# Performance work log

Measured on AMD Instinct MI355X. Metric: run time of the kernel, lower is better.

Reference implementation:

```python
import jax, jax.numpy as jnp
import numpy as np

B, T, D = 8, 2048, 512


def setup_inputs() -> dict:
    key = jax.random.key(0)
    ks = jax.random.split(key, 12)
    s = 1.0 / np.sqrt(D)
    return {
        "x": jax.random.normal(ks[0], (B, T, D), dtype=jnp.float32),
        "Wq": jax.random.normal(ks[1], (D, D), dtype=jnp.float32) * s,
        "bq": jax.random.normal(ks[2], (D,), dtype=jnp.float32) * 0.01,
        "Wk": jax.random.normal(ks[3], (D, D), dtype=jnp.float32) * s,
        "bk": jax.random.normal(ks[4], (D,), dtype=jnp.float32) * 0.01,
        "Wv": jax.random.normal(ks[5], (D, D), dtype=jnp.float32) * s,
        "bv": jax.random.normal(ks[6], (D,), dtype=jnp.float32) * 0.01,
        "Wbeta": jax.random.normal(ks[7], (1, D), dtype=jnp.float32) * s,
        "bbeta": jax.random.normal(ks[8], (1,), dtype=jnp.float32) * 0.01,
        "Wo": jax.random.normal(ks[9], (D, D), dtype=jnp.float32) * s,
        "bo": jax.random.normal(ks[10], (D,), dtype=jnp.float32) * 0.01,
    }


def _l2_normalize(v, eps=1e-12):
    # torch F.normalize(p=2, dim=-1): v / max(||v||, eps)
    n = jnp.sqrt(jnp.sum(v * v, axis=-1, keepdims=True))
    return v / jnp.maximum(n, eps)


def _deltanet(x, Wq, bq, Wk, bk, Wv, bv, Wbeta, bbeta, Wo, bo):
    Q = x @ Wq.T + bq                      # [B,T,D]
    K = _l2_normalize(x @ Wk.T + bk)       # [B,T,D], unit-norm keys
    V = x @ Wv.T + bv                      # [B,T,D]
    Beta = jax.nn.sigmoid(K @ Wbeta.T + bbeta)  # [B,T,1]

    # time-major for scan: [T,B,D] / [T,B,1]
    Qt = jnp.swapaxes(Q, 0, 1)
    Kt = jnp.swapaxes(K, 0, 1)
    Vt = jnp.swapaxes(V, 0, 1)
    Bt = jnp.swapaxes(Beta, 0, 1)

    S0 = jnp.zeros((x.shape[0], x.shape[-1], x.shape[-1]), dtype=x.dtype)

    def step(S, inp):
        q, k, v, beta = inp                 # [B,D],[B,D],[B,D],[B,1]
        Sk = jnp.einsum("bij,bj->bi", S, k)           # S k_t
        b = beta[:, :, None]                            # [B,1,1]
        # S_t = S - beta (S k) k^T + beta v k^T
        S = S - b * (Sk[:, :, None] * k[:, None, :]) + b * (v[:, :, None] * k[:, None, :])
        o = jnp.einsum("bij,bj->bi", S, q)              # o_t = S_t q_t
        return S, o

    _, Ot = jax.lax.scan(step, S0, (Qt, Kt, Vt, Bt))    # [T,B,D]
    O = jnp.swapaxes(Ot, 0, 1)                          # [B,T,D]
    return O @ Wo.T + bo


def reference(x, Wq, bq, Wk, bk, Wv, bv, Wbeta, bbeta, Wo, bo):
    return _deltanet(x, Wq, bq, Wk, bk, Wv, bv, Wbeta, bbeta, Wo, bo)
```

## Files before the change

### kernel.cpp

```cpp
#include <hip/hip_runtime.h>

#define D 512
#define T 2048
#define BATCH 8
#define M_ROWS (BATCH*T)
#define CHK 64
#define NCHB 32
#define NCHUNK 256

typedef __attribute__((ext_vector_type(8))) short short8;
typedef __attribute__((ext_vector_type(4))) float floatx4;

__device__ __forceinline__ unsigned short f2bf(float f) {
  unsigned int u = __float_as_uint(f);
  u += 0x7FFFu + ((u >> 16) & 1u);
  return (unsigned short)(u >> 16);
}
__device__ __forceinline__ float bf2f(unsigned int h) {
  return __uint_as_float(h << 16);
}
__device__ __forceinline__ float wave_allreduce(float v) {
  #pragma unroll
  for (int m = 32; m; m >>= 1) v += __shfl_xor(v, m, 64);
  return v;
}
__device__ __forceinline__ void unpack8(uint4 r, float f[8]) {
  f[0] = bf2f(r.x & 0xffffu); f[1] = bf2f(r.x >> 16);
  f[2] = bf2f(r.y & 0xffffu); f[3] = bf2f(r.y >> 16);
  f[4] = bf2f(r.z & 0xffffu); f[5] = bf2f(r.z >> 16);
  f[6] = bf2f(r.w & 0xffffu); f[7] = bf2f(r.w >> 16);
}

typedef const __attribute__((address_space(1))) void* gas_ptr;
typedef __attribute__((address_space(3))) void* lds_ptr;
__device__ __forceinline__ void gld16(const void* g, void* l) {
  __builtin_amdgcn_global_load_lds((gas_ptr)g, (lds_ptr)l, 16, 0, 0);
}

__global__ __launch_bounds__(256) void cast_all(
    const float* __restrict__ x,
    const float* __restrict__ Wq, const float* __restrict__ Wk,
    const float* __restrict__ Wv, const float* __restrict__ Wo,
    unsigned short* __restrict__ Xb, unsigned short* __restrict__ Wqb) {
  int blk = blockIdx.x;
  const float* src;
  unsigned short* dst;
  int idx;
  if (blk < 4096) {
    src = x; dst = Xb; idx = blk * 2048 + threadIdx.x * 8;
  } else {
    int b2 = blk - 4096;
    int sel = b2 >> 7;
    src = (sel == 0) ? Wq : (sel == 1) ? Wk : (sel == 2) ? Wv : Wo;
    dst = Wqb + (size_t)sel * (D * D);
    idx = (b2 & 127) * 2048 + threadIdx.x * 8;
  }
  const float4* sp = (const float4*)(src + idx);
  float4 a = sp[0], b = sp[1];
  uint4 o;
  o.x = f2bf(a.x) | ((unsigned)f2bf(a.y) << 16);
  o.y = f2bf(a.z) | ((unsigned)f2bf(a.w) << 16);
  o.z = f2bf(b.x) | ((unsigned)f2bf(b.y) << 16);
  o.w = f2bf(b.z) | ((unsigned)f2bf(b.w) << 16);
  *(uint4*)(dst + idx) = o;
}

#define BM 128
#define BN 128
#define BK 32

template<bool OUT_BF16>
__global__ __launch_bounds__(256) void gemm_nt(
    const unsigned short* __restrict__ A, const unsigned short* __restrict__ Bw,
    const float* __restrict__ bias, void* __restrict__ Cout, int M, int N, int K)
{
  __shared__ __align__(16) unsigned short As[BM * BK];
  __shared__ __align__(16) unsigned short Bs[BN * BK];
  int tid  = threadIdx.x;
  int lane = tid & 63;
  int wave = tid >> 6;
  int waveM = (wave >> 1) * 64;
  int waveN = (wave & 1) * 64;
  int lrow = lane & 15;
  int quad = lane >> 4;

  floatx4 acc[4][4];
  #pragma unroll
  for (int a_ = 0; a_ < 4; ++a_)
    #pragma unroll
    for (int b_ = 0; b_ < 4; ++b_) acc[a_][b_] = (floatx4){0.f, 0.f, 0.f, 0.f};

  const unsigned short* Ap = A  + (size_t)(blockIdx.y * BM) * K;
  const unsigned short* Bp = Bw + (size_t)(blockIdx.x * BN) * K;
  int r0 = tid >> 2;
  int c0 = (tid & 3) * 8;

  unsigned short* AsW = As + (wave << 9);
  unsigned short* BsW = Bs + (wave << 9);
  const unsigned short* ApL = Ap + (size_t)r0 * K + c0;
  const unsigned short* ApH = Ap + (size_t)(r0 + 64) * K + c0;
  const unsigned short* BpL = Bp + (size_t)r0 * K + c0;
  const unsigned short* BpH = Bp + (size_t)(r0 + 64) * K + c0;

  for (int k0 = 0; k0 < K; k0 += BK) {
    __syncthreads();
    gld16(ApL + k0, AsW);
    gld16(ApH + k0, AsW + 2048);
    gld16(BpL + k0, BsW);
    gld16(BpH + k0, BsW + 2048);
    __syncthreads();
    short8 af[4], bf[4];
    #pragma unroll
    for (int mt = 0; mt < 4; ++mt)
      af[mt] = *(const short8*)&As[(waveM + mt * 16 + lrow) * BK + quad * 8];
    #pragma unroll
    for (int nt = 0; nt < 4; ++nt)
      bf[nt] = *(const short8*)&Bs[(waveN + nt * 16 + lrow) * BK + quad * 8];
    #pragma unroll
    for (int mt = 0; mt < 4; ++mt)
      #pragma unroll
      for (int nt = 0; nt < 4; ++nt)
        acc[mt][nt] = __builtin_amdgcn_mfma_f32_16x16x32_bf16(af[mt], bf[nt], acc[mt][nt], 0, 0, 0);
  }

  int cm = blockIdx.y * BM + waveM;
  int cn = blockIdx.x * BN + waveN;
  #pragma unroll
  for (int nt = 0; nt < 4; ++nt) {
    int col = cn + nt * 16 + lrow;
    float bv = bias[col];
    #pragma unroll
    for (int mt = 0; mt < 4; ++mt) {
      #pragma unroll
      for (int r = 0; r < 4; ++r) {
        int row = cm + mt * 16 + quad * 4 + r;
        float v = acc[mt][nt][r] + bv;
        if (OUT_BF16) ((unsigned short*)Cout)[(size_t)row * N + col] = f2bf(v);
        else          ((float*)Cout)[(size_t)row * N + col] = v;
      }
    }
  }
}

__global__ __launch_bounds__(256) void gemm_qkv(
    const unsigned short* __restrict__ A, const unsigned short* __restrict__ Bw,
    const float* __restrict__ bq, const float* __restrict__ bk,
    const float* __restrict__ bv, unsigned short* __restrict__ Cout)
{
  __shared__ __align__(16) unsigned short As[BM * BK];
  __shared__ __align__(16) unsigned short Bs[BN * BK];
  const int K = D;
  int tid  = threadIdx.x;
  int lane = tid & 63;
  int wave = tid >> 6;
  int waveM = (wave >> 1) * 64;
  int waveN = (wave & 1) * 64;
  int lrow = lane & 15;
  int quad = lane >> 4;

  int mat = blockIdx.x >> 2;
  const float* bias = (mat == 0) ? bq : (mat == 1 ? bk : bv);

  floatx4 acc[4][4];
  #pragma unroll
  for (int a_ = 0; a_ < 4; ++a_)
    #pragma unroll
    for (int b_ = 0; b_ < 4; ++b_) acc[a_][b_] = (floatx4){0.f, 0.f, 0.f, 0.f};

  const unsigned short* Ap = A  + (size_t)(blockIdx.y * BM) * K;
  const unsigned short* Bp = Bw + (size_t)(blockIdx.x * BN) * K;
  int r0 = tid >> 2;
  int c0 = (tid & 3) * 8;

  unsigned short* AsW = As + (wave << 9);
  unsigned short* BsW = Bs + (wave << 9);
  const unsigned short* ApL = Ap + (size_t)r0 * K + c0;
  const unsigned short* ApH = Ap + (size_t)(r0 + 64) * K + c0;
  const unsigned short* BpL = Bp + (size_t)r0 * K + c0;
  const unsigned short* BpH = Bp + (size_t)(r0 + 64) * K + c0;

  for (int k0 = 0; k0 < K; k0 += BK) {
    __syncthreads();
    gld16(ApL + k0, AsW);
    gld16(ApH + k0, AsW + 2048);
    gld16(BpL + k0, BsW);
    gld16(BpH + k0, BsW + 2048);
    __syncthreads();
    short8 af[4], bf[4];
    #pragma unroll
    for (int mt = 0; mt < 4; ++mt)
      af[mt] = *(const short8*)&As[(waveM + mt * 16 + lrow) * BK + quad * 8];
    #pragma unroll
    for (int nt = 0; nt < 4; ++nt)
      bf[nt] = *(const short8*)&Bs[(waveN + nt * 16 + lrow) * BK + quad * 8];
    #pragma unroll
    for (int mt = 0; mt < 4; ++mt)
      #pragma unroll
      for (int nt = 0; nt < 4; ++nt)
        acc[mt][nt] = __builtin_amdgcn_mfma_f32_16x16x32_bf16(af[mt], bf[nt], acc[mt][nt], 0, 0, 0);
  }

  unsigned short* outb = Cout + (size_t)mat * ((size_t)M_ROWS * D);
  int cm = blockIdx.y * BM + waveM;
  int cnl = (blockIdx.x & 3) * BN + waveN;
  #pragma unroll
  for (int nt = 0; nt < 4; ++nt) {
    int col = cnl + nt * 16 + lrow;
    float bvv = bias[col];
    #pragma unroll
    for (int mt = 0; mt < 4; ++mt) {
      #pragma unroll
      for (int r = 0; r < 4; ++r) {
        int row = cm + mt * 16 + quad * 4 + r;
        outb[(size_t)row * D + col] = f2bf(acc[mt][nt][r] + bvv);
      }
    }
  }
}

__global__ __launch_bounds__(256) void norm_beta_kernel(
    unsigned short* __restrict__ Kb, const float* __restrict__ Wbeta,
    const float* __restrict__ bbeta, float* __restrict__ Beta)
{
  int w = blockIdx.x * 4 + (threadIdx.x >> 6);
  int lane = threadIdx.x & 63;
  unsigned short* kp = Kb + (size_t)w * D + lane * 8;
  uint4 raw = *(uint4*)kp;
  float kv[8]; unpack8(raw, kv);
  float ss = 0.f;
  #pragma unroll
  for (int m = 0; m < 8; ++m) ss += kv[m] * kv[m];
  ss = wave_allreduce(ss);
  float inv = 1.0f / fmaxf(sqrtf(ss), 1e-12f);
  const float* wb = Wbeta + lane * 8;
  float dotp = 0.f;
  #pragma unroll
  for (int m = 0; m < 8; ++m) { kv[m] *= inv; dotp += kv[m] * wb[m]; }
  uint4 o;
  o.x = f2bf(kv[0]) | ((unsigned)f2bf(kv[1]) << 16);
  o.y = f2bf(kv[2]) | ((unsigned)f2bf(kv[3]) << 16);
  o.z = f2bf(kv[4]) | ((unsigned)f2bf(kv[5]) << 16);
  o.w = f2bf(kv[6]) | ((unsigned)f2bf(kv[7]) << 16);
  *(uint4*)kp = o;
  dotp = wave_allreduce(dotp);
  if (lane == 0) Beta[w] = 1.0f / (1.0f + expf(-(dotp + bbeta[0])));
}

__global__ __launch_bounds__(256) void transpose_kv(
    const unsigned short* __restrict__ Kb, const unsigned short* __restrict__ Vb,
    unsigned short* __restrict__ KT, unsigned short* __restrict__ VT)
{
  __shared__ __align__(16) unsigned short Kc[64 * 520];
  int cb = blockIdx.x & 255, tid = threadIdx.x;
  const unsigned short* src = (blockIdx.x < 256 ? Kb : Vb) + (size_t)cb * 64 * 512;
  unsigned short* dst = (blockIdx.x < 256 ? KT : VT) + (size_t)cb * 32768;
  #pragma unroll
  for (int it = 0; it < 16; ++it) {
    int e = it * 2048 + tid * 8;
    int row = e >> 9, col = e & 511;
    *(uint4*)&Kc[row * 520 + col] = *(const uint4*)&src[row * 512 + col];
  }
  __syncthreads();
  #pragma unroll
  for (int it = 0; it < 16; ++it) {
    int e = it * 2048 + tid * 8;
    int dk = e >> 6, t0 = e & 63;
    uint4 o;
    unsigned short tv[8];
    #pragma unroll
    for (int u = 0; u < 8; ++u) tv[u] = Kc[(t0 + u) * 520 + dk];
    o.x = tv[0] | ((unsigned)tv[1] << 16);
    o.y = tv[2] | ((unsigned)tv[3] << 16);
    o.z = tv[4] | ((unsigned)tv[5] << 16);
    o.w = tv[6] | ((unsigned)tv[7] << 16);
    *(uint4*)&dst[e] = o;
  }
}

__global__ __launch_bounds__(256) void gram_kernel(
    const unsigned short* __restrict__ Qb, const unsigned short* __restrict__ Kb,
    const float* __restrict__ Beta, float* __restrict__ Abuf,
    unsigned short* __restrict__ Msb)
{
  int cb = blockIdx.x, tid = threadIdx.x, lane = tid & 63, w = tid >> 6;
  int lr = lane & 15, quad = lane >> 4;
  const unsigned short* kc = Kb + (size_t)cb * 64 * 512;
  const unsigned short* qc = Qb + (size_t)cb * 64 * 512;
  floatx4 accK[4], accQ[4];
  #pragma unroll
  for (int nt = 0; nt < 4; ++nt) { accK[nt] = (floatx4){0,0,0,0}; accQ[nt] = (floatx4){0,0,0,0}; }
  #pragma unroll
  for (int ks = 0; ks < 16; ++ks) {
    short8 ak = *(const short8*)&kc[(w * 16 + lr) * 512 + ks * 32 + quad * 8];
    short8 aq = *(const short8*)&qc[(w * 16 + lr) * 512 + ks * 32 + quad * 8];
    short8 bk[4];
    #pragma unroll
    for (int nt = 0; nt < 4; ++nt)
      bk[nt] = *(const short8*)&kc[(nt * 16 + lr) * 512 + ks * 32 + quad * 8];
    #pragma unroll
    for (int nt = 0; nt < 4; ++nt) {
      accK[nt] = __builtin_amdgcn_mfma_f32_16x16x32_bf16(ak, bk[nt], accK[nt], 0, 0, 0);
      accQ[nt] = __builtin_amdgcn_mfma_f32_16x16x32_bf16(aq, bk[nt], accQ[nt], 0, 0, 0);
    }
  }
  #pragma unroll
  for (int nt = 0; nt < 4; ++nt)
    #pragma unroll
    for (int r = 0; r < 4; ++r) {
      int t = w * 16 + quad * 4 + r;
      int j = nt * 16 + lr;
      float bt = Beta[cb * 64 + t];
      Abuf[(size_t)cb * 4096 + t * 64 + j] = (j < t) ? bt * accK[nt][r] : 0.f;
      Msb[(size_t)cb * 4096 + t * 64 + j]  = f2bf((j <= t) ? accQ[nt][r] : 0.f);
    }
}

__global__ __launch_bounds__(64) void tinv_kernel(
    const float* __restrict__ Abuf, const float* __restrict__ Beta,
    unsigned short* __restrict__ Tib)
{
  __shared__ float AB[64 * 64];
  __shared__ float XT[64 * 68];
  int lane = threadIdx.x;
  int cb = blockIdx.x;
  float bl = Beta[cb * 64 + lane];
  const float* Ab = Abuf + (size_t)cb * 4096;
  unsigned short* To = Tib + (size_t)cb * 4096;
  #pragma unroll
  for (int it = 0; it < 16; ++it) {
    int idx = it * 256 + lane * 4;
    *(float4*)&AB[idx] = *(const float4*)&Ab[idx];
  }
  float* Xr = XT + lane * 68;
  #pragma unroll
  for (int j = 0; j < 68; j += 4) *(float4*)&Xr[j] = (float4){0.f,0.f,0.f,0.f};
  for (int t = 0; t < 64; ++t) {
    const float* Ar = AB + t * 64;
    float p0 = 0.f, p1 = 0.f, p2 = 0.f, p3 = 0.f;
    for (int jb = 0; jb < t; jb += 4) {
      float4 xv = *(const float4*)&Xr[jb];
      float4 av = *(const float4*)&Ar[jb];
      p0 = fmaf(av.x, xv.x, p0); p1 = fmaf(av.y, xv.y, p1);
      p2 = fmaf(av.z, xv.z, p2); p3 = fmaf(av.w, xv.w, p3);
    }
    float y = ((lane == t) ? 1.f : 0.f) - (p0 + p1) - (p2 + p3);
    Xr[t] = y;
    To[t * 64 + lane] = f2bf(y * bl);
  }
}

__global__ __launch_bounds__(256) void wu_kernel(
    const unsigned short* __restrict__ Tib, const unsigned short* __restrict__ KT,
    const unsigned short* __restrict__ VT, unsigned short* __restrict__ Wneg,
    unsigned short* __restrict__ Ubar)
{
  __shared__ __align__(16) unsigned short WL[64 * 256];
  __shared__ __align__(16) unsigned short UL[64 * 256];
  int cb = blockIdx.x >> 1, half = blockIdx.x & 1;
  int tid = threadIdx.x, lane = tid & 63, w = tid >> 6;
  int lr = lane & 15, quad = lane >> 4;
  short8 af0 = *(const short8*)&Tib[(size_t)cb * 4096 + (w * 16 + lr) * 64 + quad * 8];
  short8 af1 = *(const short8*)&Tib[(size_t)cb * 4096 + (w * 16 + lr) * 64 + 32 + quad * 8];
  const unsigned short* ktc = KT + (size_t)cb * 32768 + lr * 64 + quad * 8;
  const unsigned short* vtc = VT + (size_t)cb * 32768 + lr * 64 + quad * 8;
  int tbase = w * 16 + quad * 4;
  int nt0 = half * 16;
  #pragma unroll 4
  for (int ntl = 0; ntl < 16; ++ntl) {
    int nt = nt0 + ntl;
    short8 bk0 = *(const short8*)(ktc + nt * 1024);
    short8 bk1 = *(const short8*)(ktc + nt * 1024 + 32);
    short8 bv0 = *(const short8*)(vtc + nt * 1024);
    short8 bv1 = *(const short8*)(vtc + nt * 1024 + 32);
    floatx4 z = (floatx4){0.f,0.f,0.f,0.f};
    floatx4 aw = __builtin_amdgcn_mfma_f32_16x16x32_bf16(af0, bk0, z, 0, 0, 0);
    aw = __builtin_amdgcn_mfma_f32_16x16x32_bf16(af1, bk1, aw, 0, 0, 0);
    floatx4 au = __builtin_amdgcn_mfma_f32_16x16x32_bf16(af0, bv0, z, 0, 0, 0);
    au = __builtin_amdgcn_mfma_f32_16x16x32_bf16(af1, bv1, au, 0, 0, 0);
    int bi = ntl * 2 + (lr >> 3);
    int lo = lr & 7;
    #pragma unroll
    for (int r = 0; r < 4; ++r) {
      int tt = tbase + r;
      int bis = bi ^ (tt & 7);
      WL[tt * 256 + bis * 8 + lo] = f2bf(-aw[r]);
      UL[tt * 256 + bis * 8 + lo] = f2bf(au[r]);
    }
  }
  __syncthreads();
  unsigned short* wd = Wneg + (size_t)cb * 32768 + half * 256;
  unsigned short* ud = Ubar + (size_t)cb * 32768 + half * 256;
  #pragma unroll
  for (int it = 0; it < 8; ++it) {
    int e = it * 2048 + tid * 8;
    int row = e >> 8, col = e & 255;
    int bis = (col >> 3) ^ (row & 7);
    *(uint4*)&wd[(size_t)row * 512 + col] = *(const uint4*)&WL[row * 256 + bis * 8];
    *(uint4*)&ud[(size_t)row * 512 + col] = *(const uint4*)&UL[row * 256 + bis * 8];
  }
}

__global__ __launch_bounds__(256, 1) void seq_kernel(
    const unsigned short* __restrict__ Wneg, const unsigned short* __restrict__ Qb,
    const unsigned short* __restrict__ Ubar, const unsigned short* __restrict__ Msb,
    const unsigned short* __restrict__ KT, unsigned short* __restrict__ Ob)
{
  __shared__ __align__(16) unsigned short Sb[16 * 520];
  __shared__ __align__(16) unsigned short Ut[16 * 72];
  int blk = blockIdx.x;
  int b = blk & 7, vs = blk >> 3;
  int vg0 = vs * 16;
  int tid = threadIdx.x, lane = tid & 63, w = tid >> 6;
  int lr = lane & 15, quad = lane >> 4;

  floatx4 sacc[8];
  #pragma unroll
  for (int nt = 0; nt < 8; ++nt) sacc[nt] = (floatx4){0.f,0.f,0.f,0.f};

  short8 wn[16], qf[16], kt[16], ms[2];
  unsigned short ub[4];

  auto LD_WQ = [&](int cb) {
    const unsigned short* wr = Wneg + ((size_t)cb * 64 + w * 16 + lr) * 512 + quad * 8;
    const unsigned short* qr = Qb   + ((size_t)cb * 64 + w * 16 + lr) * 512 + quad * 8;
    #pragma unroll
    for (int ks = 0; ks < 16; ++ks) {
      wn[ks] = *(const short8*)(wr + ks * 32);
      qf[ks] = *(const short8*)(qr + ks * 32);
    }
  };
  auto LD_KM = [&](int cb) {
    const unsigned short* kr = KT + (size_t)cb * 32768 + (w * 128 + lr) * 64 + quad * 8;
    #pragma unroll
    for (int nt = 0; nt < 8; ++nt) {
      kt[nt * 2 + 0] = *(const short8*)(kr + nt * 1024);
      kt[nt * 2 + 1] = *(const short8*)(kr + nt * 1024 + 32);
    }
    const unsigned short* mr = Msb + (size_t)cb * 4096 + (w * 16 + lr) * 64 + quad * 8;
    ms[0] = *(const short8*)(mr);
    ms[1] = *(const short8*)(mr + 32);
  };
  auto LD_UB = [&](int cb) {
    const unsigned short* ur = Ubar + ((size_t)cb * 64 + w * 16 + quad * 4) * 512 + vg0 + lr;
    #pragma unroll
    for (int r = 0; r < 4; ++r) ub[r] = ur[r * 512];
  };

  int cb0 = b * NCHB;
  LD_WQ(cb0); LD_KM(cb0); LD_UB(cb0);

  for (int ch = 0; ch < NCHB; ++ch) {
    int cb = cb0 + ch;
    int cbn = cb0 + (ch + 1 < NCHB ? ch + 1 : ch);
    #pragma unroll
    for (int nt = 0; nt < 8; ++nt)
      #pragma unroll
      for (int r = 0; r < 4; ++r)
        Sb[(quad * 4 + r) * 520 + w * 128 + nt * 16 + lr] = f2bf(sacc[nt][r]);
    __syncthreads();
    floatx4 du0, du1, do0, do1;
    #pragma unroll
    for (int r = 0; r < 4; ++r) du0[r] = bf2f(ub[r]);
    du1 = (floatx4){0.f,0.f,0.f,0.f};
    do0 = (floatx4){0.f,0.f,0.f,0.f};
    do1 = (floatx4){0.f,0.f,0.f,0.f};
    #pragma unroll
    for (int ks = 0; ks < 16; ++ks) {
      short8 sb = *(const short8*)&Sb[lr * 520 + ks * 32 + quad * 8];
      if (ks & 1) {
        du1 = __builtin_amdgcn_mfma_f32_16x16x32_bf16(wn[ks], sb, du1, 0, 0, 0);
        do1 = __builtin_amdgcn_mfma_f32_16x16x32_bf16(qf[ks], sb, do1, 0, 0, 0);
      } else {
        du0 = __builtin_amdgcn_mfma_f32_16x16x32_bf16(wn[ks], sb, du0, 0, 0, 0);
        do0 = __builtin_amdgcn_mfma_f32_16x16x32_bf16(qf[ks], sb, do0, 0, 0, 0);
      }
    }
    #pragma unroll
    for (int r = 0; r < 4; ++r)
      Ut[lr * 72 + w * 16 + quad * 4 + r] = f2bf(du0[r] + du1[r]);
    LD_WQ(cbn);
    LD_UB(cbn);
    __syncthreads();
    short8 a2_0 = *(const short8*)&Ut[lr * 72 + quad * 8];
    short8 a2_1 = *(const short8*)&Ut[lr * 72 + 32 + quad * 8];
    do0 = __builtin_amdgcn_mfma_f32_16x16x32_bf16(ms[0], a2_0, do0, 0, 0, 0);
    do1 = __builtin_amdgcn_mfma_f32_16x16x32_bf16(ms[1], a2_1, do1, 0, 0, 0);
    #pragma unroll
    for (int nt = 0; nt < 8; ++nt) {
      sacc[nt] = __builtin_amdgcn_mfma_f32_16x16x32_bf16(a2_0, kt[nt * 2 + 0], sacc[nt], 0, 0, 0);
      sacc[nt] = __builtin_amdgcn_mfma_f32_16x16x32_bf16(a2_1, kt[nt * 2 + 1], sacc[nt], 0, 0, 0);
    }
    {
      unsigned short* ob = Ob + ((size_t)cb * 64 + w * 16 + quad * 4) * 512 + vg0 + lr;
      #pragma unroll
      for (int r = 0; r < 4; ++r) ob[r * 512] = f2bf(do0[r] + do1[r]);
    }
    LD_KM(cbn);
  }
}

extern "C" void kernel_launch(void* const* d_in, const int* in_sizes, int n_in,
                              void* d_out, int out_size, void* d_ws, size_t ws_size,
                              hipStream_t stream) {
  const float* x     = (const float*)d_in[0];
  const float* Wq    = (const float*)d_in[1];
  const float* bq    = (const float*)d_in[2];
  const float* Wk    = (const float*)d_in[3];
  const float* bk    = (const float*)d_in[4];
  const float* Wv    = (const float*)d_in[5];
  const float* bv    = (const float*)d_in[6];
  const float* Wbeta = (const float*)d_in[7];
  const float* bbeta = (const float*)d_in[8];
  const float* Wo    = (const float*)d_in[9];
  const float* bo    = (const float*)d_in[10];

  const size_t NE = (size_t)M_ROWS * D;
  const size_t DD = (size_t)D * D;
  unsigned short* Qb  = (unsigned short*)d_ws;
  unsigned short* Kb  = Qb + NE;
  unsigned short* Vb  = Kb + NE;
  unsigned short* Xb  = Vb + NE;
  unsigned short* Wqb = Xb + NE;
  unsigned short* Wkb = Wqb + DD;
  unsigned short* Wvb = Wkb + DD;
  unsigned short* Wob = Wvb + DD;
  float* Beta = (float*)(Wob + DD);
  unsigned short* KT  = (unsigned short*)(Beta + M_ROWS);
  float* Abuf = (float*)(KT + NE);
  unsigned short* Msb = (unsigned short*)(Abuf + (size_t)NCHUNK * 4096);
  unsigned short* Tib = Msb + (size_t)NCHUNK * 4096;
  unsigned short* VT  = Tib + (size_t)NCHUNK * 4096;

  cast_all<<<4608, 256, 0, stream>>>(x, Wq, Wk, Wv, Wo, Xb, Wqb);

  dim3 gq(12, M_ROWS / BM);
  gemm_qkv<<<gq, 256, 0, stream>>>(Xb, Wqb, bq, bk, bv, Qb);

  norm_beta_kernel<<<M_ROWS / 4, 256, 0, stream>>>(Kb, Wbeta, bbeta, Beta);

  transpose_kv<<<2 * NCHUNK, 256, 0, stream>>>(Kb, Vb, KT, VT);
  gram_kernel<<<NCHUNK, 256, 0, stream>>>(Qb, Kb, Beta, Abuf, Msb);
  tinv_kernel<<<NCHUNK, 64, 0, stream>>>(Abuf, Beta, Tib);
  wu_kernel<<<2 * NCHUNK, 256, 0, stream>>>(Tib, KT, VT, Xb, Kb);

  seq_kernel<<<NCHUNK, 256, 0, stream>>>(Xb, Qb, Kb, Msb, KT, Vb);

  dim3 gg(D / BN, M_ROWS / BM);
  gemm_nt<false><<<gg, 256, 0, stream>>>(Vb, Wob, bo, (float*)d_out, M_ROWS, D, D);
}
```

Measured before the change: 424.7 us.

## Fuse key normalization into transpose and triangular inverse into gram kernel

```diff
diff --git a/kernel.cpp b/kernel.cpp
--- a/kernel.cpp
+++ b/kernel.cpp
@@ -218,47 +218,51 @@
   }
 }
 
-__global__ __launch_bounds__(256) void norm_beta_kernel(
-    unsigned short* __restrict__ Kb, const float* __restrict__ Wbeta,
-    const float* __restrict__ bbeta, float* __restrict__ Beta)
-{
-  int w = blockIdx.x * 4 + (threadIdx.x >> 6);
-  int lane = threadIdx.x & 63;
-  unsigned short* kp = Kb + (size_t)w * D + lane * 8;
-  uint4 raw = *(uint4*)kp;
-  float kv[8]; unpack8(raw, kv);
-  float ss = 0.f;
-  #pragma unroll
-  for (int m = 0; m < 8; ++m) ss += kv[m] * kv[m];
-  ss = wave_allreduce(ss);
-  float inv = 1.0f / fmaxf(sqrtf(ss), 1e-12f);
-  const float* wb = Wbeta + lane * 8;
-  float dotp = 0.f;
-  #pragma unroll
-  for (int m = 0; m < 8; ++m) { kv[m] *= inv; dotp += kv[m] * wb[m]; }
-  uint4 o;
-  o.x = f2bf(kv[0]) | ((unsigned)f2bf(kv[1]) << 16);
-  o.y = f2bf(kv[2]) | ((unsigned)f2bf(kv[3]) << 16);
-  o.z = f2bf(kv[4]) | ((unsigned)f2bf(kv[5]) << 16);
-  o.w = f2bf(kv[6]) | ((unsigned)f2bf(kv[7]) << 16);
-  *(uint4*)kp = o;
-  dotp = wave_allreduce(dotp);
-  if (lane == 0) Beta[w] = 1.0f / (1.0f + expf(-(dotp + bbeta[0])));
-}
-
-__global__ __launch_bounds__(256) void transpose_kv(
-    const unsigned short* __restrict__ Kb, const unsigned short* __restrict__ Vb,
+__global__ __launch_bounds__(256) void transpose_norm(
+    unsigned short* __restrict__ Kb, const unsigned short* __restrict__ Vb,
+    const float* __restrict__ Wbeta, const float* __restrict__ bbeta,
+    float* __restrict__ Beta,
     unsigned short* __restrict__ KT, unsigned short* __restrict__ VT)
 {
   __shared__ __align__(16) unsigned short Kc[64 * 520];
   int cb = blockIdx.x & 255, tid = threadIdx.x;
-  const unsigned short* src = (blockIdx.x < 256 ? Kb : Vb) + (size_t)cb * 64 * 512;
-  unsigned short* dst = (blockIdx.x < 256 ? KT : VT) + (size_t)cb * 32768;
-  #pragma unroll
-  for (int it = 0; it < 16; ++it) {
-    int e = it * 2048 + tid * 8;
-    int row = e >> 9, col = e & 511;
-    *(uint4*)&Kc[row * 520 + col] = *(const uint4*)&src[row * 512 + col];
+  bool isK = blockIdx.x < 256;
+  unsigned short* dst = (isK ? KT : VT) + (size_t)cb * 32768;
+  if (isK) {
+    int lane = tid & 63, w = tid >> 6;
+    const float* wb = Wbeta + lane * 8;
+    #pragma unroll
+    for (int i = 0; i < 16; ++i) {
+      int row = w * 16 + i;
+      unsigned short* kp = Kb + ((size_t)cb * 64 + row) * 512 + lane * 8;
+      uint4 raw = *(uint4*)kp;
+      float kv[8]; unpack8(raw, kv);
+      float ss = 0.f;
+      #pragma unroll
+      for (int m = 0; m < 8; ++m) ss += kv[m] * kv[m];
+      ss = wave_allreduce(ss);
+      float inv = 1.0f / fmaxf(sqrtf(ss), 1e-12f);
+      float dotp = 0.f;
+      #pragma unroll
+      for (int m = 0; m < 8; ++m) { kv[m] *= inv; dotp += kv[m] * wb[m]; }
+      uint4 o;
+      o.x = f2bf(kv[0]) | ((unsigned)f2bf(kv[1]) << 16);
+      o.y = f2bf(kv[2]) | ((unsigned)f2bf(kv[3]) << 16);
+      o.z = f2bf(kv[4]) | ((unsigned)f2bf(kv[5]) << 16);
+      o.w = f2bf(kv[6]) | ((unsigned)f2bf(kv[7]) << 16);
+      *(uint4*)kp = o;
+      *(uint4*)&Kc[row * 520 + lane * 8] = o;
+      dotp = wave_allreduce(dotp);
+      if (lane == 0) Beta[cb * 64 + row] = 1.0f / (1.0f + expf(-(dotp + bbeta[0])));
+    }
+  } else {
+    const unsigned short* src = Vb + (size_t)cb * 64 * 512;
+    #pragma unroll
+    for (int it = 0; it < 16; ++it) {
+      int e = it * 2048 + tid * 8;
+      int row = e >> 9, col = e & 511;
+      *(uint4*)&Kc[row * 520 + col] = *(const uint4*)&src[row * 512 + col];
+    }
   }
   __syncthreads();
   #pragma unroll
@@ -277,13 +281,18 @@
   }
 }
 
-__global__ __launch_bounds__(256) void gram_kernel(
+__global__ __launch_bounds__(256) void gram_tinv(
     const unsigned short* __restrict__ Qb, const unsigned short* __restrict__ Kb,
-    const float* __restrict__ Beta, float* __restrict__ Abuf,
-    unsigned short* __restrict__ Msb)
+    const float* __restrict__ Beta, unsigned short* __restrict__ Msb,
+    unsigned short* __restrict__ Tib)
 {
+  __shared__ float Af[64 * 68];
+  __shared__ float XT[64 * 68];
   int cb = blockIdx.x, tid = threadIdx.x, lane = tid & 63, w = tid >> 6;
   int lr = lane & 15, quad = lane >> 4;
+  if (tid < 64) {
+    *(float4*)&Af[tid * 68 + 64] = (float4){0.f,0.f,0.f,0.f};
+  }
   const unsigned short* kc = Kb + (size_t)cb * 64 * 512;
   const unsigned short* qc = Qb + (size_t)cb * 64 * 512;
   floatx4 accK[4], accQ[4];
@@ -310,42 +319,30 @@
       int t = w * 16 + quad * 4 + r;
       int j = nt * 16 + lr;
       float bt = Beta[cb * 64 + t];
-      Abuf[(size_t)cb * 4096 + t * 64 + j] = (j < t) ? bt * accK[nt][r] : 0.f;
-      Msb[(size_t)cb * 4096 + t * 64 + j]  = f2bf((j <= t) ? accQ[nt][r] : 0.f);
-    }
-}
-
-__global__ __launch_bounds__(64) void tinv_kernel(
-    const float* __restrict__ Abuf, const float* __restrict__ Beta,
-    unsigned short* __restrict__ Tib)
-{
-  __shared__ float AB[64 * 64];
-  __shared__ float XT[64 * 68];
-  int lane = threadIdx.x;
-  int cb = blockIdx.x;
-  float bl = Beta[cb * 64 + lane];
-  const float* Ab = Abuf + (size_t)cb * 4096;
-  unsigned short* To = Tib + (size_t)cb * 4096;
-  #pragma unroll
-  for (int it = 0; it < 16; ++it) {
-    int idx = it * 256 + lane * 4;
-    *(float4*)&AB[idx] = *(const float4*)&Ab[idx];
-  }
-  float* Xr = XT + lane * 68;
-  #pragma unroll
-  for (int j = 0; j < 68; j += 4) *(float4*)&Xr[j] = (float4){0.f,0.f,0.f,0.f};
-  for (int t = 0; t < 64; ++t) {
-    const float* Ar = AB + t * 64;
-    float p0 = 0.f, p1 = 0.f, p2 = 0.f, p3 = 0.f;
-    for (int jb = 0; jb < t; jb += 4) {
-      float4 xv = *(const float4*)&Xr[jb];
-      float4 av = *(const float4*)&Ar[jb];
-      p0 = fmaf(av.x, xv.x, p0); p1 = fmaf(av.y, xv.y, p1);
-      p2 = fmaf(av.z, xv.z, p2); p3 = fmaf(av.w, xv.w, p3);
-    }
-    float y = ((lane == t) ? 1.f : 0.f) - (p0 + p1) - (p2 + p3);
-    Xr[t] = y;
-    To[t * 64 + lane] = f2bf(y * bl);
+      Af[t * 68 + j] = (j < t) ? bt * accK[nt][r] : 0.f;
+      Msb[(size_t)cb * 4096 + t * 64 + j] = f2bf((j <= t) ? accQ[nt][r] : 0.f);
+    }
+  __syncthreads();
+  if (tid < 64) {
+    int l = tid;
+    float bl = Beta[cb * 64 + l];
+    unsigned short* To = Tib + (size_t)cb * 4096;
+    float* Xr = XT + l * 68;
+    #pragma unroll
+    for (int j = 0; j < 68; j += 4) *(float4*)&Xr[j] = (float4){0.f,0.f,0.f,0.f};
+    for (int t = 0; t < 64; ++t) {
+      const float* Ar = Af + t * 68;
+      float p0 = 0.f, p1 = 0.f, p2 = 0.f, p3 = 0.f;
+      for (int jb = 0; jb < t; jb += 4) {
+        float4 xv = *(const float4*)&Xr[jb];
+        float4 av = *(const float4*)&Ar[jb];
+        p0 = fmaf(av.x, xv.x, p0); p1 = fmaf(av.y, xv.y, p1);
+        p2 = fmaf(av.z, xv.z, p2); p3 = fmaf(av.w, xv.w, p3);
+      }
+      float y = ((l == t) ? 1.f : 0.f) - (p0 + p1) - (p2 + p3);
+      Xr[t] = y;
+      To[t * 64 + l] = f2bf(y * bl);
+    }
   }
 }
 
@@ -536,11 +533,8 @@
   dim3 gq(12, M_ROWS / BM);
   gemm_qkv<<<gq, 256, 0, stream>>>(Xb, Wqb, bq, bk, bv, Qb);
 
-  norm_beta_kernel<<<M_ROWS / 4, 256, 0, stream>>>(Kb, Wbeta, bbeta, Beta);
-
-  transpose_kv<<<2 * NCHUNK, 256, 0, stream>>>(Kb, Vb, KT, VT);
-  gram_kernel<<<NCHUNK, 256, 0, stream>>>(Qb, Kb, Beta, Abuf, Msb);
-  tinv_kernel<<<NCHUNK, 64, 0, stream>>>(Abuf, Beta, Tib);
+  transpose_norm<<<2 * NCHUNK, 256, 0, stream>>>(Kb, Vb, Wbeta, bbeta, Beta, KT, VT);
+  gram_tinv<<<NCHUNK, 256, 0, stream>>>(Qb, Kb, Beta, Msb, Tib);
   wu_kernel<<<2 * NCHUNK, 256, 0, stream>>>(Tib, KT, VT, Xb, Kb);
 
   seq_kernel<<<NCHUNK, 256, 0, stream>>>(Xb, Qb, Kb, Msb, KT, Vb);
```

Measured after the change: 426.7 us. About the same (+0.5%).
